# Kernel tuning notes

Hardware: AMD Instinct MI355X
Metric: run time of the kernel (lower is better)

Reference implementation:

```python
import jax, jax.numpy as jnp
import numpy as np

FORGET_BIAS = 1.0  # tf LSTMCell default

def _lstm_step(c, h, xt, W, b):
    # tf LSTMCell: gates = [x, h] @ W + b, split order (i, j, f, o)
    gates = jnp.concatenate([xt, h], axis=-1) @ W + b
    i, j, f, o = jnp.split(gates, 4, axis=-1)
    c_new = c * jax.nn.sigmoid(f + FORGET_BIAS) + jax.nn.sigmoid(i) * jnp.tanh(j)
    h_new = jnp.tanh(c_new) * jax.nn.sigmoid(o)
    return c_new, h_new

def setup_inputs() -> dict:
    key = jax.random.key(0)
    k1, k2, k3 = jax.random.split(key, 3)
    B, T, H = 512, 1024, 64
    x = jax.random.normal(k1, (B, T, 1), dtype=jnp.float32)
    W1 = jax.random.normal(k2, (1 + H, 4 * H), dtype=jnp.float32) * 0.1
    b1 = jnp.zeros((4 * H,), dtype=jnp.float32)
    W2 = jax.random.normal(k3, (H + 1, 4 * 1), dtype=jnp.float32) * 0.1
    b2 = jnp.zeros((4,), dtype=jnp.float32)
    return {"x": x, "W1": W1, "b1": b1, "W2": W2, "b2": b2}

def reference(x, W1, b1, W2, b2):
    B, T, _ = x.shape
    H = W1.shape[1] // 4
    xs = jnp.swapaxes(x, 0, 1)  # [T, B, 1]

    def step(carry, xt):
        c1, h1, c2, h2 = carry
        c1, h1 = _lstm_step(c1, h1, xt, W1, b1)   # layer 1: in=1, hidden=64
        c2, h2 = _lstm_step(c2, h2, h1, W2, b2)   # layer 2: in=64, hidden=1
        return (c1, h1, c2, h2), h2

    init = (jnp.zeros((B, H), x.dtype), jnp.zeros((B, H), x.dtype),
            jnp.zeros((B, 1), x.dtype), jnp.zeros((B, 1), x.dtype))
    _, ys = jax.lax.scan(step, init, xs)  # ys: [T, B, 1]
    return jnp.swapaxes(ys, 0, 1)  # [B, T, 1]
```

## Files before the change

### kernel.cpp

```cpp
#include <hip/hip_runtime.h>


#define TT 1024

__device__ __forceinline__ float fsig(float x) {
    return __builtin_amdgcn_rcpf(1.f + __expf(-x));
}
__device__ __forceinline__ float ftanh(float x) {
    return 1.f - 2.f * __builtin_amdgcn_rcpf(1.f + __expf(2.f * x));
}

template <int Ctrl, int Rmask>
__device__ __forceinline__ float dpp_add(float x) {
    int t = __builtin_amdgcn_update_dpp(0, __float_as_int(x), Ctrl, Rmask, 0xf, true);
    return x + __int_as_float(t);
}
__device__ __forceinline__ float wave_sum64(float x) {
    x = dpp_add<0x111, 0xf>(x);
    x = dpp_add<0x112, 0xf>(x);
    x = dpp_add<0x114, 0xf>(x);
    x = dpp_add<0x118, 0xf>(x);
    x = dpp_add<0x142, 0xa>(x);
    x = dpp_add<0x143, 0xc>(x);
    return x;
}

__device__ __forceinline__ float bcast(float v, int l) {
    return __uint_as_float(__builtin_amdgcn_readlane(__float_as_uint(v), l));
}

__global__ __attribute__((amdgpu_waves_per_eu(1, 1))) __launch_bounds__(128)
void lstm2_kernel(
    const float* __restrict__ x,
    const float* __restrict__ W1,
    const float* __restrict__ b1,
    const float* __restrict__ W2,
    const float* __restrict__ b2,
    float* __restrict__ y)
{
    __shared__ __align__(16) float xs[TT];
    __shared__ __align__(16) float gls[2][4][64];
    __shared__ __align__(16) float dls[2][4];

    const int tid  = threadIdx.x;
    const int lane = tid & 63;
    const int wid  = tid >> 6;
    const int b    = blockIdx.x;

    {
        const float4* src = (const float4*)(x + (size_t)b * TT);
        float4* dst = (float4*)xs;
        dst[tid]       = src[tid];
        dst[128 + tid] = src[128 + tid];
    }

    const int ga = wid << 1, gb = ga | 1;
    const int ca = (ga << 6) | lane;
    const int cb = (gb << 6) | lane;

    float wxa = W1[ca], wxb = W1[cb];
    float bsa = b1[ca], bsb = b1[cb];
    float wha[64], whb[64];
#pragma unroll
    for (int j = 0; j < 64; ++j) {
        wha[j] = W1[(j + 1) * 256 + ca];
        whb[j] = W1[(j + 1) * 256 + cb];
    }
#define PIN4(A, B, C, D) asm volatile("" : "+v"(A), "+v"(B), "+v"(C), "+v"(D))
#pragma unroll
    for (int j = 0; j < 64; j += 4) {
        PIN4(wha[j], wha[j + 1], wha[j + 2], wha[j + 3]);
        PIN4(whb[j], whb[j + 1], whb[j + 2], whb[j + 3]);
    }
    PIN4(wxa, wxb, bsa, bsb);
#undef PIN4

    const float w2ga = W2[lane * 4 + ga];
    const float w2gb = W2[lane * 4 + gb];
    const float w2h0 = W2[256], w2h1 = W2[257], w2h2 = W2[258], w2h3 = W2[259];
    const float b20 = b2[0], b21 = b2[1], b22 = b2[2], b23 = b2[3];

    const float L2E = 1.4426950408889634f;
    const float mma = -L2E;
    const float kka = (ga == 2) ? -L2E : 0.f;
    const float mmb = (gb == 1) ? 2.f * L2E : -L2E;
    const float aab = (gb == 1) ? 1.f : 0.f;
    const float bbb = (gb == 1) ? -2.f : 1.f;

    float c1 = 0.f, hv = 0.f;
    float c2v = 0.f, h2v = 0.f;
    float* yrow = y + (size_t)b * TT;

    __syncthreads();

#define STEP(PAR, XT, DOL2, YI) { \
        float a0 = fmaf((XT), wxa, bsa), a1 = 0.f, a2 = 0.f, a3 = 0.f; \
        float e0 = fmaf((XT), wxb, bsb), e1 = 0.f, e2 = 0.f, e3 = 0.f; \
        _Pragma("unroll") \
        for (int j = 0; j < 64; j += 4) { \
            const float s0 = bcast(hv, j + 0), s1 = bcast(hv, j + 1); \
            const float s2 = bcast(hv, j + 2), s3 = bcast(hv, j + 3); \
            a0 = fmaf(s0, wha[j + 0], a0); e0 = fmaf(s0, whb[j + 0], e0); \
            a1 = fmaf(s1, wha[j + 1], a1); e1 = fmaf(s1, whb[j + 1], e1); \
            a2 = fmaf(s2, wha[j + 2], a2); e2 = fmaf(s2, whb[j + 2], e2); \
            a3 = fmaf(s3, wha[j + 3], a3); e3 = fmaf(s3, whb[j + 3], e3); \
        } \
        const float pa = (a0 + a1) + (a2 + a3); \
        const float pb = (e0 + e1) + (e2 + e3); \
        const float da = wave_sum64(hv * w2ga);    \
        const float db = wave_sum64(hv * w2gb); \
        const float acta = __builtin_amdgcn_rcpf(1.f + exp2f(fmaf(mma, pa, kka))); \
        const float actb = fmaf(bbb, __builtin_amdgcn_rcpf(1.f + exp2f(mmb * pb)), aab); \
        gls[PAR][ga][lane] = acta; \
        gls[PAR][gb][lane] = actb; \
        if (lane == 63) { dls[PAR][ga] = da; dls[PAR][gb] = db; } \
        __syncthreads();           \
        { \
            const float i_ = gls[PAR][0][lane], j_ = gls[PAR][1][lane]; \
            const float f_ = gls[PAR][2][lane], o_ = gls[PAR][3][lane]; \
            c1 = fmaf(c1, f_, i_ * j_); \
            hv = ftanh(c1) * o_; \
        } \
        if (wid == 0 && (DOL2)) {   \
            const float4 d4 = *(const float4*)(&dls[PAR][0]); \
            const float i2 = fsig (fmaf(h2v, w2h0, d4.x) + b20); \
            const float j2 = ftanh(fmaf(h2v, w2h1, d4.y) + b21); \
            const float f2 = fsig (fmaf(h2v, w2h2, d4.z) + b22 + 1.f); \
            const float o2 = fsig (fmaf(h2v, w2h3, d4.w) + b23); \
            c2v = fmaf(c2v, f2, i2 * j2); \
            h2v = ftanh(c2v) * o2; \
            if (lane == 0) yrow[YI] = h2v; \
        } }

    for (int t = 0; t < TT; t += 4) {
        const float4 x4 = *(const float4*)(xs + t);
        STEP(0, x4.x, t > 0, t - 1)
        STEP(1, x4.y, true,  t + 0)
        STEP(0, x4.z, true,  t + 1)
        STEP(1, x4.w, true,  t + 2)
    }
#undef STEP

    {
        const float da = wave_sum64(hv * w2ga);
        const float db = wave_sum64(hv * w2gb);
        if (lane == 63) { dls[0][ga] = da; dls[0][gb] = db; }
        __syncthreads();
        if (tid == 0) {
            const float4 d4 = *(const float4*)(&dls[0][0]);
            const float i2 = fsig (fmaf(h2v, w2h0, d4.x) + b20);
            const float j2 = ftanh(fmaf(h2v, w2h1, d4.y) + b21);
            const float f2 = fsig (fmaf(h2v, w2h2, d4.z) + b22 + 1.f);
            const float o2 = fsig (fmaf(h2v, w2h3, d4.w) + b23);
            c2v = fmaf(c2v, f2, i2 * j2);
            h2v = ftanh(c2v) * o2;
            yrow[TT - 1] = h2v;
        }
    }
}

extern "C" void kernel_launch(void* const* d_in, const int* in_sizes, int n_in,
                              void* d_out, int out_size, void* d_ws, size_t ws_size,
                              hipStream_t stream) {
    const float* x  = (const float*)d_in[0];
    const float* W1 = (const float*)d_in[1];
    const float* b1 = (const float*)d_in[2];
    const float* W2 = (const float*)d_in[3];
    const float* b2 = (const float*)d_in[4];
    float* y = (float*)d_out;
    lstm2_kernel<<<512, 128, 0, stream>>>(x, W1, b1, W2, b2, y);
}
```

Before: 749.2 us.

## Offload layer-2 LSTM to a dedicated third wave pipelined with layer 1

Adds a third wavefront per block that computes the layer-2 cell from a double-buffered shared copy of h1, one step behind layer 1. The two layer-1 waves no longer do the wave reductions or the layer-2 activations inside their serial recurrence. In exchange every barrier now spans three waves, and the block uses more resources per CU.

```diff
diff --git a/kernel.cpp b/kernel.cpp
--- a/kernel.cpp
+++ b/kernel.cpp
@@ -29,7 +29,7 @@
     return __uint_as_float(__builtin_amdgcn_readlane(__float_as_uint(v), l));
 }
 
-__global__ __attribute__((amdgpu_waves_per_eu(1, 1))) __launch_bounds__(128)
+__global__ __attribute__((amdgpu_waves_per_eu(1, 1))) __launch_bounds__(192)
 void lstm2_kernel(
     const float* __restrict__ x,
     const float* __restrict__ W1,
@@ -40,60 +40,55 @@
 {
     __shared__ __align__(16) float xs[TT];
     __shared__ __align__(16) float gls[2][4][64];
-    __shared__ __align__(16) float dls[2][4];
+    __shared__ __align__(16) float h1s[2][64];
 
     const int tid  = threadIdx.x;
     const int lane = tid & 63;
     const int wid  = tid >> 6;
     const int b    = blockIdx.x;
 
-    {
+    if (tid < 128) {
         const float4* src = (const float4*)(x + (size_t)b * TT);
         float4* dst = (float4*)xs;
         dst[tid]       = src[tid];
         dst[128 + tid] = src[128 + tid];
     }
 
-    const int ga = wid << 1, gb = ga | 1;
-    const int ca = (ga << 6) | lane;
-    const int cb = (gb << 6) | lane;
+    float* yrow = y + (size_t)b * TT;
 
-    float wxa = W1[ca], wxb = W1[cb];
-    float bsa = b1[ca], bsb = b1[cb];
-    float wha[64], whb[64];
+    if (wid < 2) {
+        const int ga = wid << 1, gb = ga | 1;
+        const int ca = (ga << 6) | lane;
+        const int cb = (gb << 6) | lane;
+
+        float wxa = W1[ca], wxb = W1[cb];
+        float bsa = b1[ca], bsb = b1[cb];
+        float wha[64], whb[64];
 #pragma unroll
-    for (int j = 0; j < 64; ++j) {
-        wha[j] = W1[(j + 1) * 256 + ca];
-        whb[j] = W1[(j + 1) * 256 + cb];
-    }
+        for (int j = 0; j < 64; ++j) {
+            wha[j] = W1[(j + 1) * 256 + ca];
+            whb[j] = W1[(j + 1) * 256 + cb];
+        }
 #define PIN4(A, B, C, D) asm volatile("" : "+v"(A), "+v"(B), "+v"(C), "+v"(D))
 #pragma unroll
-    for (int j = 0; j < 64; j += 4) {
-        PIN4(wha[j], wha[j + 1], wha[j + 2], wha[j + 3]);
-        PIN4(whb[j], whb[j + 1], whb[j + 2], whb[j + 3]);
-    }
-    PIN4(wxa, wxb, bsa, bsb);
+        for (int j = 0; j < 64; j += 4) {
+            PIN4(wha[j], wha[j + 1], wha[j + 2], wha[j + 3]);
+            PIN4(whb[j], whb[j + 1], whb[j + 2], whb[j + 3]);
+        }
+        PIN4(wxa, wxb, bsa, bsb);
 #undef PIN4
 
-    const float w2ga = W2[lane * 4 + ga];
-    const float w2gb = W2[lane * 4 + gb];
-    const float w2h0 = W2[256], w2h1 = W2[257], w2h2 = W2[258], w2h3 = W2[259];
-    const float b20 = b2[0], b21 = b2[1], b22 = b2[2], b23 = b2[3];
+        const float L2E = 1.4426950408889634f;
+        const float mma = -L2E;
+        const float kka = (ga == 2) ? -L2E : 0.f;
+        const float mmb = (gb == 1) ? 2.f * L2E : -L2E;
+        const float aab = (gb == 1) ? 1.f : 0.f;
+        const float bbb = (gb == 1) ? -2.f : 1.f;
 
-    const float L2E = 1.4426950408889634f;
-    const float mma = -L2E;
-    const float kka = (ga == 2) ? -L2E : 0.f;
-    const float mmb = (gb == 1) ? 2.f * L2E : -L2E;
-    const float aab = (gb == 1) ? 1.f : 0.f;
-    const float bbb = (gb == 1) ? -2.f : 1.f;
+        float c1 = 0.f, hv = 0.f;
+        __syncthreads();
 
-    float c1 = 0.f, hv = 0.f;
-    float c2v = 0.f, h2v = 0.f;
-    float* yrow = y + (size_t)b * TT;
-
-    __syncthreads();
-
-#define STEP(PAR, XT, DOL2, YI) { \
+#define STEP(PAR, XT) { \
         float a0 = fmaf((XT), wxa, bsa), a1 = 0.f, a2 = 0.f, a3 = 0.f; \
         float e0 = fmaf((XT), wxb, bsb), e1 = 0.f, e2 = 0.f, e3 = 0.f; \
         _Pragma("unroll") \
@@ -107,54 +102,70 @@
         } \
         const float pa = (a0 + a1) + (a2 + a3); \
         const float pb = (e0 + e1) + (e2 + e3); \
-        const float da = wave_sum64(hv * w2ga);    \
-        const float db = wave_sum64(hv * w2gb); \
         const float acta = __builtin_amdgcn_rcpf(1.f + exp2f(fmaf(mma, pa, kka))); \
         const float actb = fmaf(bbb, __builtin_amdgcn_rcpf(1.f + exp2f(mmb * pb)), aab); \
         gls[PAR][ga][lane] = acta; \
         gls[PAR][gb][lane] = actb; \
-        if (lane == 63) { dls[PAR][ga] = da; dls[PAR][gb] = db; } \
         __syncthreads();           \
         { \
             const float i_ = gls[PAR][0][lane], j_ = gls[PAR][1][lane]; \
             const float f_ = gls[PAR][2][lane], o_ = gls[PAR][3][lane]; \
             c1 = fmaf(c1, f_, i_ * j_); \
             hv = ftanh(c1) * o_; \
-        } \
-        if (wid == 0 && (DOL2)) {   \
-            const float4 d4 = *(const float4*)(&dls[PAR][0]); \
-            const float i2 = fsig (fmaf(h2v, w2h0, d4.x) + b20); \
-            const float j2 = ftanh(fmaf(h2v, w2h1, d4.y) + b21); \
-            const float f2 = fsig (fmaf(h2v, w2h2, d4.z) + b22 + 1.f); \
-            const float o2 = fsig (fmaf(h2v, w2h3, d4.w) + b23); \
-            c2v = fmaf(c2v, f2, i2 * j2); \
-            h2v = ftanh(c2v) * o2; \
-            if (lane == 0) yrow[YI] = h2v; \
+            if (wid == 0) h1s[PAR][lane] = hv;    \
         } }
 
-    for (int t = 0; t < TT; t += 4) {
-        const float4 x4 = *(const float4*)(xs + t);
-        STEP(0, x4.x, t > 0, t - 1)
-        STEP(1, x4.y, true,  t + 0)
-        STEP(0, x4.z, true,  t + 1)
-        STEP(1, x4.w, true,  t + 2)
-    }
+        for (int t = 0; t < TT; t += 4) {
+            const float4 x4 = *(const float4*)(xs + t);
+            STEP(0, x4.x)
+            STEP(1, x4.y)
+            STEP(0, x4.z)
+            STEP(1, x4.w)
+        }
 #undef STEP
+        __syncthreads();
+    } else {
+        const float4 w2g4 = *(const float4*)(W2 + lane * 4);
+        const float w2h0 = W2[256], w2h1 = W2[257], w2h2 = W2[258], w2h3 = W2[259];
+        const float b20 = b2[0], b21 = b2[1], b22 = b2[2], b23 = b2[3];
+        float c2 = 0.f, h2 = 0.f;
+        __syncthreads();
 
-    {
-        const float da = wave_sum64(hv * w2ga);
-        const float db = wave_sum64(hv * w2gb);
-        if (lane == 63) { dls[0][ga] = da; dls[0][gb] = db; }
+        for (int t = 0; t < TT; ++t) {
+            __syncthreads();
+            if (t > 0) {
+                const float hv = h1s[(t - 1) & 1][lane];
+                const float d0 = wave_sum64(hv * w2g4.x);
+                const float d1 = wave_sum64(hv * w2g4.y);
+                const float d2 = wave_sum64(hv * w2g4.z);
+                const float d3 = wave_sum64(hv * w2g4.w);
+                if (lane == 63) {
+                    const float i2 = fsig (fmaf(h2, w2h0, d0) + b20);
+                    const float j2 = ftanh(fmaf(h2, w2h1, d1) + b21);
+                    const float f2 = fsig (fmaf(h2, w2h2, d2) + b22 + 1.f);
+                    const float o2 = fsig (fmaf(h2, w2h3, d3) + b23);
+                    c2 = fmaf(c2, f2, i2 * j2);
+                    h2 = ftanh(c2) * o2;
+                    yrow[t - 1] = h2;
+                }
+            }
+        }
         __syncthreads();
-        if (tid == 0) {
-            const float4 d4 = *(const float4*)(&dls[0][0]);
-            const float i2 = fsig (fmaf(h2v, w2h0, d4.x) + b20);
-            const float j2 = ftanh(fmaf(h2v, w2h1, d4.y) + b21);
-            const float f2 = fsig (fmaf(h2v, w2h2, d4.z) + b22 + 1.f);
-            const float o2 = fsig (fmaf(h2v, w2h3, d4.w) + b23);
-            c2v = fmaf(c2v, f2, i2 * j2);
-            h2v = ftanh(c2v) * o2;
-            yrow[TT - 1] = h2v;
+        {
+            const float hv = h1s[(TT - 1) & 1][lane];
+            const float d0 = wave_sum64(hv * w2g4.x);
+            const float d1 = wave_sum64(hv * w2g4.y);
+            const float d2 = wave_sum64(hv * w2g4.z);
+            const float d3 = wave_sum64(hv * w2g4.w);
+            if (lane == 63) {
+                const float i2 = fsig (fmaf(h2, w2h0, d0) + b20);
+                const float j2 = ftanh(fmaf(h2, w2h1, d1) + b21);
+                const float f2 = fsig (fmaf(h2, w2h2, d2) + b22 + 1.f);
+                const float o2 = fsig (fmaf(h2, w2h3, d3) + b23);
+                c2 = fmaf(c2, f2, i2 * j2);
+                h2 = ftanh(c2) * o2;
+                yrow[TT - 1] = h2;
+            }
         }
     }
 }
@@ -168,5 +179,5 @@
     const float* W2 = (const float*)d_in[3];
     const float* b2 = (const float*)d_in[4];
     float* y = (float*)d_out;
-    lstm2_kernel<<<512, 128, 0, stream>>>(x, W1, b1, W2, b2, y);
+    lstm2_kernel<<<512, 192, 0, stream>>>(x, W1, b1, W2, b2, y);
 }
```

Measured after the change: 1.130 ms. +50.8%, slower.
